# Kernel optimization log

Hardware: AMD Instinct MI355X
Metric: run time of the kernel (lower is better)

Reference implementation:

```python
import jax, jax.numpy as jnp
import numpy as np

N = 100000
E = 1600000
D = 128      # input feature dim
H = 128      # hidden_channels
O = 2        # out_channels
NEG_SLOPE = 0.2
EPS = 1e-16  # PyG softmax denominator epsilon


def gat_conv(x, src, dst, W_src, W_dst, att_src, att_dst, bias):
    """PyG GATConv, heads=1, add_self_loops=False, concat=True."""
    xs = x @ W_src                      # [N, C]
    xd = x @ W_dst                      # [N, C]
    a_s = xs @ att_src                  # [N]
    a_d = xd @ att_dst                  # [N]
    e = jax.nn.leaky_relu(a_s[src] + a_d[dst], NEG_SLOPE)   # [E]
    # segment softmax over edges grouped by destination node
    m = jax.ops.segment_max(e, dst, num_segments=N)          # [N]
    m = jnp.where(jnp.isfinite(m), m, 0.0)
    ex = jnp.exp(e - m[dst])                                  # [E]
    denom = jax.ops.segment_sum(ex, dst, num_segments=N)      # [N]
    alpha = ex / (denom[dst] + EPS)                            # [E]
    msg = alpha[:, None] * xs[src]                             # [E, C]
    out = jax.ops.segment_sum(msg, dst, num_segments=N)       # [N, C]
    return out + bias


def setup_inputs() -> dict:
    key = jax.random.key(0)
    ks = jax.random.split(key, 14)
    s = lambda k, shape, fan: jax.random.normal(k, shape, jnp.float32) * (1.0 / np.sqrt(fan))
    x = jax.random.normal(ks[0], (N, D), jnp.float32)
    edge_index = jax.random.randint(ks[1], (2, E), 0, N, dtype=jnp.int32)
    return {
        "x": x,
        "edge_index": edge_index,
        "W1s": s(ks[2], (D, H), D), "W1d": s(ks[3], (D, H), D),
        "a1s": s(ks[4], (H,), H),   "a1d": s(ks[5], (H,), H),
        "b1": jnp.zeros((H,), jnp.float32),
        "W2s": s(ks[6], (H, H), H), "W2d": s(ks[7], (H, H), H),
        "a2s": s(ks[8], (H,), H),   "a2d": s(ks[9], (H,), H),
        "b2": jnp.zeros((H,), jnp.float32),
        "Wl": s(ks[10], (H, O), H), "bl": jnp.zeros((O,), jnp.float32),
    }


def reference(x, edge_index, W1s, W1d, a1s, a1d, b1, W2s, W2d, a2s, a2d, b2, Wl, bl):
    src, dst = edge_index[0], edge_index[1]
    h = jax.nn.relu(gat_conv(x, src, dst, W1s, W1d, a1s, a1d, b1))
    # dropout p=0.3 is identity at inference
    h = jax.nn.relu(gat_conv(h, src, dst, W2s, W2d, a2s, a2d, b2))
    return h @ Wl + bl  # [N, O]
```

## Files before the change

kernel.cpp:

```cpp
#include <hip/hip_runtime.h>
#include <hip/hip_fp16.h>

#define NBSHIFT 8
#define BSZ     256
#define CAP     5120
#define EBLK    8192

typedef _Float16 f16x8 __attribute__((ext_vector_type(8)));
typedef float    f32x4 __attribute__((ext_vector_type(4)));

#define GEMM_LDS_BYTES (128 * 136 * 2 + 512)

__device__ __forceinline__ f16x8 cvt_dot8(float4 x0, float4 x1, const float* sv, float& adp) {
    f16x8 a;
    a[0] = (_Float16)x0.x; a[1] = (_Float16)x0.y; a[2] = (_Float16)x0.z; a[3] = (_Float16)x0.w;
    a[4] = (_Float16)x1.x; a[5] = (_Float16)x1.y; a[6] = (_Float16)x1.z; a[7] = (_Float16)x1.w;
    float4 v0 = *(const float4*)sv, v1 = *(const float4*)(sv + 4);
    adp += x0.x * v0.x + x0.y * v0.y + x0.z * v0.z + x0.w * v0.w
         + x1.x * v1.x + x1.y * v1.y + x1.z * v1.z + x1.w * v1.w;
    return a;
}

template <bool XHALF>
__device__ __forceinline__ void gemm_body(
        const void* __restrict__ Xv, const float* __restrict__ Ws,
        const float* __restrict__ Wd, const float* __restrict__ attd,
        const float* __restrict__ att,
        __half* __restrict__ Y, float* __restrict__ a_s, float* __restrict__ a_d,
        int N, int blk, char* smem) {
    _Float16 (*sWh)[136] = (_Float16(*)[136])smem;
    float* svd = (float*)(smem + 128 * 136 * 2);
    int t = threadIdx.x;
    int l = t & 63, wv = t >> 6;
    int quad = l >> 4, lm = l & 15;
    int rbase = blk * 64 + wv * 16;
    int arow = rbase + lm;
    bool rok = arow < N;

    float4 xf[8];
    f16x8  xh[4];
    if constexpr (XHALF) {
        const f16x8* xr = (const f16x8*)((const __half*)Xv + (size_t)arow * 128 + quad * 8);
        if (rok) { xh[0] = xr[0]; xh[1] = xr[4]; xh[2] = xr[8]; xh[3] = xr[12]; }
        else {
#pragma unroll
            for (int kc = 0; kc < 4; kc++)
#pragma unroll
                for (int j = 0; j < 8; j++) xh[kc][j] = (_Float16)0.f;
        }
    } else {
        const float4* xr = (const float4*)((const float*)Xv + (size_t)arow * 128 + quad * 8);
        if (rok) {
            xf[0] = xr[0];  xf[1] = xr[1];
            xf[2] = xr[8];  xf[3] = xr[9];
            xf[4] = xr[16]; xf[5] = xr[17];
            xf[6] = xr[24]; xf[7] = xr[25];
        } else {
#pragma unroll
            for (int j = 0; j < 8; j++) xf[j] = make_float4(0.f, 0.f, 0.f, 0.f);
        }
    }

    if (t < 128) {
        const float4* wr = (const float4*)&Wd[t * 128];
        const float4* ar = (const float4*)attd;
        float s = 0.f;
#pragma unroll 8
        for (int j = 0; j < 32; j++) {
            float4 w = wr[j], a = ar[j];
            s += w.x * a.x + w.y * a.y + w.z * a.z + w.w * a.w;
        }
        svd[t] = s;
    }
#pragma unroll
    for (int i = 0; i < 16; i++) {
        int gid = t + i * 256;
        int n = gid & 127, kq = gid >> 7;
        _Float16 p[4];
        p[0] = (_Float16)Ws[(kq * 4 + 0) * 128 + n];
        p[1] = (_Float16)Ws[(kq * 4 + 1) * 128 + n];
        p[2] = (_Float16)Ws[(kq * 4 + 2) * 128 + n];
        p[3] = (_Float16)Ws[(kq * 4 + 3) * 128 + n];
        *(uint2*)&sWh[n][kq * 4] = *(uint2*)p;
    }
    __syncthreads();

    float adp = 0.f;
    f16x8 af[4];
    if constexpr (XHALF) {
#pragma unroll
        for (int kc = 0; kc < 4; kc++) {
            af[kc] = xh[kc];
            const float* sv = &svd[kc * 32 + quad * 8];
#pragma unroll
            for (int j = 0; j < 8; j++) adp += (float)xh[kc][j] * sv[j];
        }
    } else {
        af[0] = cvt_dot8(xf[0], xf[1], &svd[0  + quad * 8], adp);
        af[1] = cvt_dot8(xf[2], xf[3], &svd[32 + quad * 8], adp);
        af[2] = cvt_dot8(xf[4], xf[5], &svd[64 + quad * 8], adp);
        af[3] = cvt_dot8(xf[6], xf[7], &svd[96 + quad * 8], adp);
    }

    f32x4 acc[8];
#pragma unroll
    for (int c = 0; c < 8; c++) acc[c] = (f32x4){0.f, 0.f, 0.f, 0.f};
#pragma unroll
    for (int kc = 0; kc < 4; kc++) {
        int k0 = kc * 32 + quad * 8;
#pragma unroll
        for (int c = 0; c < 8; c++) {
            f16x8 bf = *(const f16x8*)&sWh[c * 16 + lm][k0];
            acc[c] = __builtin_amdgcn_mfma_f32_16x16x32_f16(af[kc], bf, acc[c], 0, 0, 0);
        }
    }

    adp += __shfl_xor(adp, 16);
    adp += __shfl_xor(adp, 32);
    if (quad == 0 && rok) a_d[arow] = adp;

    float attc[8];
#pragma unroll
    for (int c = 0; c < 8; c++) attc[c] = att[c * 16 + lm];
#pragma unroll
    for (int r = 0; r < 4; r++) {
        int grow = rbase + quad * 4 + r;
        bool gok = grow < N;
        float p = 0.f;
#pragma unroll
        for (int c = 0; c < 8; c++) {
            if (gok) Y[(size_t)grow * 128 + c * 16 + lm] = __float2half(acc[c][r]);
            p += acc[c][r] * attc[c];
        }
        p += __shfl_xor(p, 1); p += __shfl_xor(p, 2); p += __shfl_xor(p, 4); p += __shfl_xor(p, 8);
        if (lm == 0 && gok) a_s[grow] = p;
    }
}

__global__ __launch_bounds__(256) void k_bin(
        const int* __restrict__ src, const int* __restrict__ dst, int E,
        int* __restrict__ cursor, unsigned* __restrict__ pairs) {
    __shared__ int hist[512];
    __shared__ int start[512];
    int t = threadIdx.x;
    hist[t] = 0; hist[t + 256] = 0;
    __syncthreads();
    int e00 = (int)blockIdx.x * EBLK;

#pragma unroll
    for (int ch = 0; ch < EBLK / 1024; ch++) {
        int e = e00 + ch * 1024 + t * 4;
        if (e + 3 < E) {
            int4 dv = *(const int4*)&dst[e];
            atomicAdd(&hist[dv.x >> NBSHIFT], 1);
            atomicAdd(&hist[dv.y >> NBSHIFT], 1);
            atomicAdd(&hist[dv.z >> NBSHIFT], 1);
            atomicAdd(&hist[dv.w >> NBSHIFT], 1);
        } else {
            for (int i = 0; i < 4; i++)
                if (e + i < E) atomicAdd(&hist[dst[e + i] >> NBSHIFT], 1);
        }
    }
    __syncthreads();
    if (hist[t] > 0)       start[t]       = atomicAdd(&cursor[t],       hist[t]);
    if (hist[t + 256] > 0) start[t + 256] = atomicAdd(&cursor[t + 256], hist[t + 256]);
    __syncthreads();
    hist[t] = 0; hist[t + 256] = 0;
    __syncthreads();
#pragma unroll
    for (int ch = 0; ch < EBLK / 1024; ch++) {
        int e = e00 + ch * 1024 + t * 4;
        if (e + 3 < E) {
            int4 dv = *(const int4*)&dst[e];
            int4 sv = *(const int4*)&src[e];
            int b0 = dv.x >> NBSHIFT; int r0 = atomicAdd(&hist[b0], 1);
            pairs[b0 * CAP + start[b0] + r0] = ((unsigned)(dv.x & (BSZ - 1)) << 17) | (unsigned)sv.x;
            int b1 = dv.y >> NBSHIFT; int r1 = atomicAdd(&hist[b1], 1);
            pairs[b1 * CAP + start[b1] + r1] = ((unsigned)(dv.y & (BSZ - 1)) << 17) | (unsigned)sv.y;
            int b2 = dv.z >> NBSHIFT; int r2 = atomicAdd(&hist[b2], 1);
            pairs[b2 * CAP + start[b2] + r2] = ((unsigned)(dv.z & (BSZ - 1)) << 17) | (unsigned)sv.z;
            int b3 = dv.w >> NBSHIFT; int r3 = atomicAdd(&hist[b3], 1);
            pairs[b3 * CAP + start[b3] + r3] = ((unsigned)(dv.w & (BSZ - 1)) << 17) | (unsigned)sv.w;
        } else {
            for (int i = 0; i < 4; i++) {
                if (e + i < E) {
                    int d = dst[e + i], s = src[e + i];
                    int b = d >> NBSHIFT;
                    int r = atomicAdd(&hist[b], 1);
                    pairs[b * CAP + start[b] + r] = ((unsigned)(d & (BSZ - 1)) << 17) | (unsigned)s;
                }
            }
        }
    }
}

__global__ __launch_bounds__(256, 4) void k_gemm1(
        const float* __restrict__ X, const float* __restrict__ W1s,
        const float* __restrict__ W1d, const float* __restrict__ a1d,
        const float* __restrict__ a1s,
        __half* __restrict__ Y, float* __restrict__ a_s, float* __restrict__ a_d, int N) {
    __shared__ __align__(16) char smem[GEMM_LDS_BYTES];
    gemm_body<false>(X, W1s, W1d, a1d, a1s, Y, a_s, a_d, N, blockIdx.x, smem);
}

__global__ __launch_bounds__(256, 4) void k_gemm2(
        const __half* __restrict__ X, const float* __restrict__ W2s,
        const float* __restrict__ W2d, const float* __restrict__ a2d,
        const float* __restrict__ a2s,
        __half* __restrict__ Y, float* __restrict__ a_s, float* __restrict__ a_d, int N) {
    __shared__ __align__(16) char smem[GEMM_LDS_BYTES];
    gemm_body<true>(X, W2s, W2d, a2d, a2s, Y, a_s, a_d, N, blockIdx.x, smem);
}

__global__ __launch_bounds__(256) void kB_csr(const unsigned* __restrict__ pairs,
                                              const int* __restrict__ cursor,
                                              int* __restrict__ row_start, int* __restrict__ row_end,
                                              int* __restrict__ csr_src, int N) {
    __shared__ int cnt[BSZ];
    __shared__ int cur[BSZ];
    __shared__ int sS[256];
    int b = blockIdx.x, t = threadIdx.x;
    int base = b * CAP;
    int ecnt = cursor[b];
    int nodeBase = b << NBSHIFT;
    cnt[t] = 0;
    __syncthreads();
    for (int j = t; j < ecnt; j += 256)
        atomicAdd(&cnt[pairs[base + j] >> 17], 1);
    __syncthreads();
    int c0 = cnt[t];
    sS[t] = c0; __syncthreads();
    for (int off = 1; off < 256; off <<= 1) {
        int x = (t >= off) ? sS[t - off] : 0;
        __syncthreads();
        sS[t] += x;
        __syncthreads();
    }
    int excl = sS[t] - c0;
    cur[t] = excl;
    int g = nodeBase + t;
    if (g < N) { row_start[g] = base + excl; row_end[g] = base + excl + c0; }
    __syncthreads();
    for (int j = t; j < ecnt; j += 256) {
        unsigned p = pairs[base + j];
        int r = atomicAdd(&cur[p >> 17], 1);
        csr_src[base + r] = (int)(p & 0x1FFFFu);
    }
}


__device__ __forceinline__ void fma_mix2(float& a0, float& a1, unsigned h2, float w) {
    asm("v_fma_mix_f32 %0, %1, %2, %0 op_sel_hi:[1,0,0]" : "+v"(a0) : "v"(h2), "v"(w));
    asm("v_fma_mix_f32 %0, %1, %2, %0 op_sel:[1,0,0] op_sel_hi:[1,0,0]" : "+v"(a1) : "v"(h2), "v"(w));
}

#define ACC_MIX(u, wj)  do {                                    \
    const unsigned* _w32 = (const unsigned*)&(u);               \
    fma_mix2(acc[0], acc[1], _w32[0], (wj));                    \
    fma_mix2(acc[2], acc[3], _w32[1], (wj));                    \
    fma_mix2(acc[4], acc[5], _w32[2], (wj));                    \
    fma_mix2(acc[6], acc[7], _w32[3], (wj));                    \
} while (0)

#define GATHER4(u0, u1, u2, u3, pa, pb)  do {                   \
    u0 = *(const uint4*)&xs[(size_t)(pa).x * 128 + c];          \
    u1 = *(const uint4*)&xs[(size_t)(pa).z * 128 + c];          \
    u2 = *(const uint4*)&xs[(size_t)(pb).x * 128 + c];          \
    u3 = *(const uint4*)&xs[(size_t)(pb).z * 128 + c];          \
} while (0)

#define CONSUME4(u0, u1, u2, u3, pa, pb)  do {                  \
    ACC_MIX(u0, __int_as_float((pa).y));                        \
    ACC_MIX(u1, __int_as_float((pa).w));                        \
    ACC_MIX(u2, __int_as_float((pb).y));                        \
    ACC_MIX(u3, __int_as_float((pb).w));                        \
} while (0)

template <bool HEAD>
__global__ __launch_bounds__(256, 5) void k_agg(const int* __restrict__ csr_src, const int* __restrict__ rs_,
                                                const int* __restrict__ re_,
                                                const float* __restrict__ a_s, const float* __restrict__ a_d,
                                                const __half* __restrict__ xs, const float* __restrict__ bias,
                                                const float* __restrict__ Wl, const float* __restrict__ bl,
                                                void* __restrict__ outv, int N) {
    __shared__ int2 sP[4][4][16];
    int t = threadIdx.x; int wv = t >> 6, l = t & 63;
    int q = l >> 4, es = l & 15;
    int n = blockIdx.x * 16 + wv * 4 + q;
    bool nok = n < N;
    int rs0 = 0, deg = 0;
    if (nok) { rs0 = rs_[n]; deg = re_[n] - rs0; }
    float adn = nok ? a_d[n] : 0.f;
    const int* cs = csr_src + rs0;
    int c = es * 8;

    int R = (deg + 15) >> 4;
    R = max(R, __shfl_xor(R, 16));
    R = max(R, __shfl_xor(R, 32));

    float acc[8];
#pragma unroll
    for (int k = 0; k < 8; k++) acc[k] = 0.f;
    float dnl = 0.f;
    int2 (*sq)[16] = sP[wv];
    const int2* spq = sq[q];

    for (int r = 0; r < R; ++r) {
        int i = r * 16 + es;
        int idx = 0; float w = 0.f;
        if (i < deg) {
            idx = cs[i];
            float tv = a_s[idx] + adn;
            tv = tv > 0.f ? tv : 0.2f * tv;
            w = __expf(tv);
        }
        dnl += w;
        sq[q][es] = make_int2(idx, __float_as_int(w));

        int4 pa0 = *(const int4*)&spq[0],  pb0 = *(const int4*)&spq[2];
        uint4 u00, u01, u02, u03;
        GATHER4(u00, u01, u02, u03, pa0, pb0);
        int4 pa1 = *(const int4*)&spq[4],  pb1 = *(const int4*)&spq[6];
        uint4 u10, u11, u12, u13;
        GATHER4(u10, u11, u12, u13, pa1, pb1);

        CONSUME4(u00, u01, u02, u03, pa0, pb0);
        pa0 = *(const int4*)&spq[8]; pb0 = *(const int4*)&spq[10];
        GATHER4(u00, u01, u02, u03, pa0, pb0);

        CONSUME4(u10, u11, u12, u13, pa1, pb1);
        pa1 = *(const int4*)&spq[12]; pb1 = *(const int4*)&spq[14];
        GATHER4(u10, u11, u12, u13, pa1, pb1);

        CONSUME4(u00, u01, u02, u03, pa0, pb0);
        CONSUME4(u10, u11, u12, u13, pa1, pb1);
    }

    dnl += __shfl_xor(dnl, 1);
    dnl += __shfl_xor(dnl, 2);
    dnl += __shfl_xor(dnl, 4);
    dnl += __shfl_xor(dnl, 8);
    float inv = 1.f / (dnl + 1e-16f);

    float hv[8];
    float4 b0 = *(const float4*)&bias[c];
    float4 b1 = *(const float4*)&bias[c + 4];
    float bb[8] = {b0.x, b0.y, b0.z, b0.w, b1.x, b1.y, b1.z, b1.w};
#pragma unroll
    for (int k = 0; k < 8; k++) {
        float v = acc[k] * inv + bb[k];
        hv[k] = v > 0.f ? v : 0.f;
    }

    if (HEAD) {
        float p0 = 0.f, p1 = 0.f;
#pragma unroll
        for (int k = 0; k < 8; k++) {
            p0 += hv[k] * Wl[2 * (c + k)];
            p1 += hv[k] * Wl[2 * (c + k) + 1];
        }
        p0 += __shfl_xor(p0, 1); p0 += __shfl_xor(p0, 2);
        p0 += __shfl_xor(p0, 4); p0 += __shfl_xor(p0, 8);
        p1 += __shfl_xor(p1, 1); p1 += __shfl_xor(p1, 2);
        p1 += __shfl_xor(p1, 4); p1 += __shfl_xor(p1, 8);
        if (es == 0 && nok) {
            float* out = (float*)outv;
            out[2 * n]     = p0 + bl[0];
            out[2 * n + 1] = p1 + bl[1];
        }
    } else {
        if (nok) {
            __half* hout = (__half*)outv;
            __half hb[8];
#pragma unroll
            for (int k = 0; k < 8; k++) hb[k] = __float2half(hv[k]);
            *(uint4*)&hout[(size_t)n * 128 + c] = *(uint4*)hb;
        }
    }
}


extern "C" void kernel_launch(void* const* d_in, const int* in_sizes, int n_in,
                              void* d_out, int out_size, void* d_ws, size_t ws_size,
                              hipStream_t stream) {
    const float* x   = (const float*)d_in[0];
    const int*   ei  = (const int*)d_in[1];
    const float* W1s = (const float*)d_in[2];
    const float* W1d = (const float*)d_in[3];
    const float* a1s = (const float*)d_in[4];
    const float* a1d = (const float*)d_in[5];
    const float* b1  = (const float*)d_in[6];
    const float* W2s = (const float*)d_in[7];
    const float* W2d = (const float*)d_in[8];
    const float* a2s = (const float*)d_in[9];
    const float* a2d = (const float*)d_in[10];
    const float* b2  = (const float*)d_in[11];
    const float* Wl  = (const float*)d_in[12];
    const float* bl  = (const float*)d_in[13];
    float* out = (float*)d_out;

    int N = in_sizes[0] / 128;
    int E = in_sizes[1] / 2;
    const int* srcA = ei;
    const int* dstA = ei + E;
    int NB = (N + BSZ - 1) >> NBSHIFT;

    __half* xs = (__half*)d_ws;
    __half* h  = xs + (size_t)N * 128;
    float* as_ = (float*)(h + (size_t)N * 128);
    float* ad_ = as_ + N;
    int* row_start = (int*)(ad_ + N);
    int* row_end   = row_start + N;
    int* csr_src   = row_end + N;
    int* cursor    = csr_src + (size_t)NB * CAP;
    unsigned* pairs = (unsigned*)h;

    int gb = (N + 63) / 64;
    int EB = (E + EBLK - 1) / EBLK;
    int ab = (N + 15) / 16;

    hipMemsetAsync(cursor, 0, (size_t)NB * 4, stream);

    k_bin<<<EB, 256, 0, stream>>>(srcA, dstA, E, cursor, pairs);

    k_gemm1<<<gb, 256, 0, stream>>>(x, W1s, W1d, a1d, a1s, xs, as_, ad_, N);

    kB_csr<<<NB, 256, 0, stream>>>(pairs, cursor, row_start, row_end, csr_src, N);

    k_agg<false><<<ab, 256, 0, stream>>>(csr_src, row_start, row_end, as_, ad_, xs, b1, nullptr, nullptr, h, N);

    k_gemm2<<<gb, 256, 0, stream>>>(h, W2s, W2d, a2d, a2s, xs, as_, ad_, N);

    k_agg<true><<<ab, 256, 0, stream>>>(csr_src, row_start, row_end, as_, ad_, xs, b2, Wl, bl, out, N);
}
```

Before: 327.5 us.

## Merge edge binning into GEMM1 launch and hand-schedule gather loads in aggregation

The edge-binning kernel is folded into the first GEMM kernel as extra blocks, so the binning and the projection GEMM run concurrently in one launch with no kernel boundary between them. The aggregation kernel now issues its feature gathers as inline-asm global loads with explicit s_waitcnt counters, keeping more loads in flight before each consume. Its occupancy hint drops from 5 to 4 waves to leave room for the extra live registers. Volatile asm and sched barriers limit the compiler's freedom, and the binning blocks now share the GEMM's larger LDS allocation, which may lower their occupancy.

```diff
diff --git a/kernel.cpp b/kernel.cpp
--- a/kernel.cpp
+++ b/kernel.cpp
@@ -137,69 +137,71 @@
     }
 }
 
-__global__ __launch_bounds__(256) void k_bin(
-        const int* __restrict__ src, const int* __restrict__ dst, int E,
-        int* __restrict__ cursor, unsigned* __restrict__ pairs) {
-    __shared__ int hist[512];
-    __shared__ int start[512];
-    int t = threadIdx.x;
-    hist[t] = 0; hist[t + 256] = 0;
-    __syncthreads();
-    int e00 = (int)blockIdx.x * EBLK;
-
-#pragma unroll
-    for (int ch = 0; ch < EBLK / 1024; ch++) {
-        int e = e00 + ch * 1024 + t * 4;
-        if (e + 3 < E) {
-            int4 dv = *(const int4*)&dst[e];
-            atomicAdd(&hist[dv.x >> NBSHIFT], 1);
-            atomicAdd(&hist[dv.y >> NBSHIFT], 1);
-            atomicAdd(&hist[dv.z >> NBSHIFT], 1);
-            atomicAdd(&hist[dv.w >> NBSHIFT], 1);
-        } else {
-            for (int i = 0; i < 4; i++)
-                if (e + i < E) atomicAdd(&hist[dst[e + i] >> NBSHIFT], 1);
-        }
-    }
-    __syncthreads();
-    if (hist[t] > 0)       start[t]       = atomicAdd(&cursor[t],       hist[t]);
-    if (hist[t + 256] > 0) start[t + 256] = atomicAdd(&cursor[t + 256], hist[t + 256]);
-    __syncthreads();
-    hist[t] = 0; hist[t + 256] = 0;
-    __syncthreads();
-#pragma unroll
-    for (int ch = 0; ch < EBLK / 1024; ch++) {
-        int e = e00 + ch * 1024 + t * 4;
-        if (e + 3 < E) {
-            int4 dv = *(const int4*)&dst[e];
-            int4 sv = *(const int4*)&src[e];
-            int b0 = dv.x >> NBSHIFT; int r0 = atomicAdd(&hist[b0], 1);
-            pairs[b0 * CAP + start[b0] + r0] = ((unsigned)(dv.x & (BSZ - 1)) << 17) | (unsigned)sv.x;
-            int b1 = dv.y >> NBSHIFT; int r1 = atomicAdd(&hist[b1], 1);
-            pairs[b1 * CAP + start[b1] + r1] = ((unsigned)(dv.y & (BSZ - 1)) << 17) | (unsigned)sv.y;
-            int b2 = dv.z >> NBSHIFT; int r2 = atomicAdd(&hist[b2], 1);
-            pairs[b2 * CAP + start[b2] + r2] = ((unsigned)(dv.z & (BSZ - 1)) << 17) | (unsigned)sv.z;
-            int b3 = dv.w >> NBSHIFT; int r3 = atomicAdd(&hist[b3], 1);
-            pairs[b3 * CAP + start[b3] + r3] = ((unsigned)(dv.w & (BSZ - 1)) << 17) | (unsigned)sv.w;
-        } else {
-            for (int i = 0; i < 4; i++) {
-                if (e + i < E) {
-                    int d = dst[e + i], s = src[e + i];
-                    int b = d >> NBSHIFT;
-                    int r = atomicAdd(&hist[b], 1);
-                    pairs[b * CAP + start[b] + r] = ((unsigned)(d & (BSZ - 1)) << 17) | (unsigned)s;
-                }
-            }
-        }
-    }
-}
-
-__global__ __launch_bounds__(256, 4) void k_gemm1(
+__global__ __launch_bounds__(256, 4) void k_fuse1(
         const float* __restrict__ X, const float* __restrict__ W1s,
         const float* __restrict__ W1d, const float* __restrict__ a1d,
         const float* __restrict__ a1s,
-        __half* __restrict__ Y, float* __restrict__ a_s, float* __restrict__ a_d, int N) {
+        __half* __restrict__ Y, float* __restrict__ a_s, float* __restrict__ a_d, int N, int gb,
+        const int* __restrict__ src, const int* __restrict__ dst, int E,
+        int* __restrict__ cursor, unsigned* __restrict__ pairs) {
     __shared__ __align__(16) char smem[GEMM_LDS_BYTES];
+    int t = threadIdx.x;
+
+    if ((int)blockIdx.x >= gb) {
+        int* hist  = (int*)smem;
+        int* start = hist + 512;
+        hist[t] = 0; hist[t + 256] = 0;
+        __syncthreads();
+        int e00 = ((int)blockIdx.x - gb) * EBLK;
+
+#pragma unroll
+        for (int ch = 0; ch < EBLK / 1024; ch++) {
+            int e = e00 + ch * 1024 + t * 4;
+            if (e + 3 < E) {
+                int4 dv = *(const int4*)&dst[e];
+                atomicAdd(&hist[dv.x >> NBSHIFT], 1);
+                atomicAdd(&hist[dv.y >> NBSHIFT], 1);
+                atomicAdd(&hist[dv.z >> NBSHIFT], 1);
+                atomicAdd(&hist[dv.w >> NBSHIFT], 1);
+            } else {
+                for (int i = 0; i < 4; i++)
+                    if (e + i < E) atomicAdd(&hist[dst[e + i] >> NBSHIFT], 1);
+            }
+        }
+        __syncthreads();
+        if (hist[t] > 0)       start[t]       = atomicAdd(&cursor[t],       hist[t]);
+        if (hist[t + 256] > 0) start[t + 256] = atomicAdd(&cursor[t + 256], hist[t + 256]);
+        __syncthreads();
+        hist[t] = 0; hist[t + 256] = 0;
+        __syncthreads();
+#pragma unroll
+        for (int ch = 0; ch < EBLK / 1024; ch++) {
+            int e = e00 + ch * 1024 + t * 4;
+            if (e + 3 < E) {
+                int4 dv = *(const int4*)&dst[e];
+                int4 sv = *(const int4*)&src[e];
+                int b0 = dv.x >> NBSHIFT; int r0 = atomicAdd(&hist[b0], 1);
+                pairs[b0 * CAP + start[b0] + r0] = ((unsigned)(dv.x & (BSZ - 1)) << 17) | (unsigned)sv.x;
+                int b1 = dv.y >> NBSHIFT; int r1 = atomicAdd(&hist[b1], 1);
+                pairs[b1 * CAP + start[b1] + r1] = ((unsigned)(dv.y & (BSZ - 1)) << 17) | (unsigned)sv.y;
+                int b2 = dv.z >> NBSHIFT; int r2 = atomicAdd(&hist[b2], 1);
+                pairs[b2 * CAP + start[b2] + r2] = ((unsigned)(dv.z & (BSZ - 1)) << 17) | (unsigned)sv.z;
+                int b3 = dv.w >> NBSHIFT; int r3 = atomicAdd(&hist[b3], 1);
+                pairs[b3 * CAP + start[b3] + r3] = ((unsigned)(dv.w & (BSZ - 1)) << 17) | (unsigned)sv.w;
+            } else {
+                for (int i = 0; i < 4; i++) {
+                    if (e + i < E) {
+                        int d = dst[e + i], s = src[e + i];
+                        int b = d >> NBSHIFT;
+                        int r = atomicAdd(&hist[b], 1);
+                        pairs[b * CAP + start[b] + r] = ((unsigned)(d & (BSZ - 1)) << 17) | (unsigned)s;
+                    }
+                }
+            }
+        }
+        return;
+    }
+
     gemm_body<false>(X, W1s, W1d, a1d, a1s, Y, a_s, a_d, N, blockIdx.x, smem);
 }
 
@@ -249,24 +251,32 @@
 }
 
 
-__device__ __forceinline__ void fma_mix2(float& a0, float& a1, unsigned h2, float w) {
-    asm("v_fma_mix_f32 %0, %1, %2, %0 op_sel_hi:[1,0,0]" : "+v"(a0) : "v"(h2), "v"(w));
-    asm("v_fma_mix_f32 %0, %1, %2, %0 op_sel:[1,0,0] op_sel_hi:[1,0,0]" : "+v"(a1) : "v"(h2), "v"(w));
+__device__ __forceinline__ void fma_mix2v(float& a0, float& a1, unsigned h2, float w) {
+    asm volatile("v_fma_mix_f32 %0, %1, %2, %0 op_sel_hi:[1,0,0]" : "+v"(a0) : "v"(h2), "v"(w));
+    asm volatile("v_fma_mix_f32 %0, %1, %2, %0 op_sel:[1,0,0] op_sel_hi:[1,0,0]" : "+v"(a1) : "v"(h2), "v"(w));
 }
 
 #define ACC_MIX(u, wj)  do {                                    \
-    const unsigned* _w32 = (const unsigned*)&(u);               \
-    fma_mix2(acc[0], acc[1], _w32[0], (wj));                    \
-    fma_mix2(acc[2], acc[3], _w32[1], (wj));                    \
-    fma_mix2(acc[4], acc[5], _w32[2], (wj));                    \
-    fma_mix2(acc[6], acc[7], _w32[3], (wj));                    \
+    unsigned _w0 = (u).x, _w1 = (u).y, _w2 = (u).z, _w3 = (u).w; \
+    fma_mix2v(acc[0], acc[1], _w0, (wj));                       \
+    fma_mix2v(acc[2], acc[3], _w1, (wj));                       \
+    fma_mix2v(acc[4], acc[5], _w2, (wj));                       \
+    fma_mix2v(acc[6], acc[7], _w3, (wj));                       \
 } while (0)
 
-#define GATHER4(u0, u1, u2, u3, pa, pb)  do {                   \
-    u0 = *(const uint4*)&xs[(size_t)(pa).x * 128 + c];          \
-    u1 = *(const uint4*)&xs[(size_t)(pa).z * 128 + c];          \
-    u2 = *(const uint4*)&xs[(size_t)(pb).x * 128 + c];          \
-    u3 = *(const uint4*)&xs[(size_t)(pb).z * 128 + c];          \
+#define GLOAD(u, sidx)  do {                                                        \
+    const __half* _p = xs + (size_t)(unsigned)(sidx) * 128 + c;                     \
+    asm volatile("global_load_dwordx4 %0, %1, off" : "=&v"(u) : "v"(_p) : "memory"); \
+} while (0)
+
+#define GBATCH(u0, u1, u2, u3, pa, pb)  do {                    \
+    GLOAD(u0, (pa).x); GLOAD(u1, (pa).z);                       \
+    GLOAD(u2, (pb).x); GLOAD(u3, (pb).z);                       \
+} while (0)
+
+#define WAITN(nn)  do {                                         \
+    asm volatile("s_waitcnt vmcnt(" #nn ")" ::: "memory");      \
+    __builtin_amdgcn_sched_barrier(0);                          \
 } while (0)
 
 #define CONSUME4(u0, u1, u2, u3, pa, pb)  do {                  \
@@ -277,13 +287,13 @@
 } while (0)
 
 template <bool HEAD>
-__global__ __launch_bounds__(256, 5) void k_agg(const int* __restrict__ csr_src, const int* __restrict__ rs_,
+__global__ __launch_bounds__(256, 4) void k_agg(const int* __restrict__ csr_src, const int* __restrict__ rs_,
                                                 const int* __restrict__ re_,
                                                 const float* __restrict__ a_s, const float* __restrict__ a_d,
                                                 const __half* __restrict__ xs, const float* __restrict__ bias,
                                                 const float* __restrict__ Wl, const float* __restrict__ bl,
                                                 void* __restrict__ outv, int N) {
-    __shared__ int2 sP[4][4][16];
+    __shared__ __align__(16) int2 sP[4][4][16];
     int t = threadIdx.x; int wv = t >> 6, l = t & 63;
     int q = l >> 4, es = l & 15;
     int n = blockIdx.x * 16 + wv * 4 + q;
@@ -303,7 +313,7 @@
     for (int k = 0; k < 8; k++) acc[k] = 0.f;
     float dnl = 0.f;
     int2 (*sq)[16] = sP[wv];
-    const int2* spq = sq[q];
+    const int4* spq4 = (const int4*)sq[q];
 
     for (int r = 0; r < R; ++r) {
         int i = r * 16 + es;
@@ -317,23 +327,27 @@
         dnl += w;
         sq[q][es] = make_int2(idx, __float_as_int(w));
 
-        int4 pa0 = *(const int4*)&spq[0],  pb0 = *(const int4*)&spq[2];
-        uint4 u00, u01, u02, u03;
-        GATHER4(u00, u01, u02, u03, pa0, pb0);
-        int4 pa1 = *(const int4*)&spq[4],  pb1 = *(const int4*)&spq[6];
-        uint4 u10, u11, u12, u13;
-        GATHER4(u10, u11, u12, u13, pa1, pb1);
-
-        CONSUME4(u00, u01, u02, u03, pa0, pb0);
-        pa0 = *(const int4*)&spq[8]; pb0 = *(const int4*)&spq[10];
-        GATHER4(u00, u01, u02, u03, pa0, pb0);
-
-        CONSUME4(u10, u11, u12, u13, pa1, pb1);
-        pa1 = *(const int4*)&spq[12]; pb1 = *(const int4*)&spq[14];
-        GATHER4(u10, u11, u12, u13, pa1, pb1);
-
-        CONSUME4(u00, u01, u02, u03, pa0, pb0);
-        CONSUME4(u10, u11, u12, u13, pa1, pb1);
+        int4 pA0 = spq4[0], pB0 = spq4[1];
+        int4 pA1 = spq4[2], pB1 = spq4[3];
+        uint4 u00, u01, u02, u03, u10, u11, u12, u13;
+        GBATCH(u00, u01, u02, u03, pA0, pB0);
+        GBATCH(u10, u11, u12, u13, pA1, pB1);
+        int4 pA2 = spq4[4], pB2 = spq4[5];
+        int4 pA3 = spq4[6], pB3 = spq4[7];
+
+        WAITN(4);
+        CONSUME4(u00, u01, u02, u03, pA0, pB0);
+        GBATCH(u00, u01, u02, u03, pA2, pB2);
+
+        WAITN(4);
+        CONSUME4(u10, u11, u12, u13, pA1, pB1);
+        GBATCH(u10, u11, u12, u13, pA3, pB3);
+
+        WAITN(4);
+        CONSUME4(u00, u01, u02, u03, pA2, pB2);
+
+        WAITN(0);
+        CONSUME4(u10, u11, u12, u13, pA3, pB3);
     }
 
     dnl += __shfl_xor(dnl, 1);
@@ -421,9 +435,8 @@
 
     hipMemsetAsync(cursor, 0, (size_t)NB * 4, stream);
 
-    k_bin<<<EB, 256, 0, stream>>>(srcA, dstA, E, cursor, pairs);
-
-    k_gemm1<<<gb, 256, 0, stream>>>(x, W1s, W1d, a1d, a1s, xs, as_, ad_, N);
+    k_fuse1<<<gb + EB, 256, 0, stream>>>(x, W1s, W1d, a1d, a1s, xs, as_, ad_, N, gb,
+                                         srcA, dstA, E, cursor, pairs);
 
     kB_csr<<<NB, 256, 0, stream>>>(pairs, cursor, row_start, row_end, csr_src, N);
 
```

New measurement: 315.5 us. -3.7%, faster.
